# Performance work log

Measured on AMD Instinct MI355X. Metric: run time of the kernel, lower is better.

## Reference

```python
import jax, jax.numpy as jnp
import numpy as np

B, L, D, C = 1, 512, 128, 128  # batch, length, input_dim, channel_dim


def _layernorm(x, w, b, eps=1e-5):
    mu = jnp.mean(x, axis=-1, keepdims=True)
    var = jnp.var(x, axis=-1, keepdims=True)
    return (x - mu) * jax.lax.rsqrt(var + eps) * w + b


def setup_inputs() -> dict:
    key = jax.random.key(0)
    ks = jax.random.split(key, 12)
    s = 0.05  # weight scale ~ xavier for d=128
    f32 = jnp.float32
    return {
        "z": jax.random.normal(ks[0], (B, L, L, D), f32),
        "ln_in_w": jnp.ones((D,), f32), "ln_in_b": jnp.zeros((D,), f32),
        "Wga": jax.random.normal(ks[1], (D, C), f32) * s, "bga": jnp.zeros((C,), f32),
        "Wla": jax.random.normal(ks[2], (D, C), f32) * s, "bla": jnp.zeros((C,), f32),
        "Wgb": jax.random.normal(ks[3], (D, C), f32) * s, "bgb": jnp.zeros((C,), f32),
        "Wlb": jax.random.normal(ks[4], (D, C), f32) * s, "blb": jnp.zeros((C,), f32),
        "ln_o_w": jnp.ones((C,), f32), "ln_o_b": jnp.zeros((C,), f32),
        "Wgo": jax.random.normal(ks[5], (D, D), f32) * s, "bgo": jnp.zeros((D,), f32),
        "Wlo": jax.random.normal(ks[6], (C, D), f32) * s, "blo": jnp.zeros((D,), f32),
    }


def reference(z, ln_in_w, ln_in_b, Wga, bga, Wla, bla, Wgb, bgb, Wlb, blb,
              ln_o_w, ln_o_b, Wgo, bgo, Wlo, blo):
    # z: [B, L, L, D]
    zn = _layernorm(z, ln_in_w, ln_in_b)
    a = jax.nn.sigmoid(zn @ Wga + bga) * (zn @ Wla + bla)   # [B,L,L,C]
    b = jax.nn.sigmoid(zn @ Wgb + bgb) * (zn @ Wlb + blb)   # [B,L,L,C]
    # triangular update (axis=1): per-channel L x L matmul
    # k[b,i,j,c] = sum_m a[b,i,m,c] * b[b,m,j,c]
    k = jnp.einsum('bimc,bmjc->bijc', a, b)
    out = jax.nn.sigmoid(zn @ Wgo + bgo) * (_layernorm(k, ln_o_w, ln_o_b) @ Wlo + blo)
    return out
```

## Files before the change

### kernel.cpp

```cpp
#include <hip/hip_runtime.h>

typedef unsigned short u16;
typedef __attribute__((ext_vector_type(8))) short bf16x8;
typedef __attribute__((ext_vector_type(4))) float f32x4;

#define L_ 512
#define D_ 128
#define LL_ (512*512)
#define LP_ 136
#define TP_ 72

#define WT_OFF 0
#define B2_OFF 98304
#define ZN_OFF (B2_OFF + 1536)
#define AT2_OFF (ZN_OFF + 128*LL_)
#define BT2_OFF (AT2_OFF + 128*LL_)
#define KT2_OFF (BT2_OFF + 128*LL_)
#define WS2_NEED_BYTES ((size_t)(KT2_OFF + 128*LL_) * 2)
#define AT1_OFF (B2_OFF + 1536)
#define BT1_OFF (AT1_OFF + 128*LL_)
#define KT1_OFF (BT1_OFF + 128*LL_)

union U16x8 { uint4 u4; bf16x8 v; u16 s[8]; };
union U16x4 { ushort4 v; u16 s[4]; };

__device__ __forceinline__ u16 f2bf(float f){
  union { float f; unsigned int i; } w; w.f = f;
  unsigned int r = w.i + 0x7FFFu + ((w.i >> 16) & 1u);
  return (u16)(r >> 16);
}
__device__ __forceinline__ float sigm(float x){
  return 1.0f / (1.0f + __expf(-x));
}

__global__ __launch_bounds__(256) void conv_kernel(
    const float* __restrict__ Wga, const float* __restrict__ Wla,
    const float* __restrict__ Wgb, const float* __restrict__ Wlb,
    const float* __restrict__ Wgo, const float* __restrict__ Wlo,
    const float* __restrict__ lnw, const float* __restrict__ lnb,
    const float* __restrict__ onw, const float* __restrict__ onb,
    const float* __restrict__ bga, const float* __restrict__ bla,
    const float* __restrict__ bgb, const float* __restrict__ blb,
    const float* __restrict__ bgo, const float* __restrict__ blo,
    u16* __restrict__ wt, float* __restrict__ bias2)
{
  if (blockIdx.x < 384){
    int idx = blockIdx.x*256 + threadIdx.x;
    int w = idx >> 14, rem = idx & 16383, n = rem >> 7, k = rem & 127;
    const float* src;
    switch (w){
      case 0: src = Wga; break; case 1: src = Wla; break; case 2: src = Wgb; break;
      case 3: src = Wlb; break; case 4: src = Wgo; break; default: src = Wlo;
    }
    float sc = (w == 5) ? onw[k] : lnw[k];
    wt[idx] = f2bf(src[k*128 + n] * sc);
  } else {
    int j = (blockIdx.x - 384)*256 + threadIdx.x;
    int w = j >> 7, n = j & 127;
    const float* src; const float* bs;
    switch (w){
      case 0: src = Wga; bs = bga; break; case 1: src = Wla; bs = bla; break;
      case 2: src = Wgb; bs = bgb; break; case 3: src = Wlb; bs = blb; break;
      case 4: src = Wgo; bs = bgo; break; default: src = Wlo; bs = blo;
    }
    const float* lb = (w == 5) ? onb : lnb;
    float acc = bs[n];
    for (int k = 0; k < 128; ++k) acc += lb[k] * src[k*128 + n];
    bias2[j] = acc;
  }
}

__global__ __launch_bounds__(256) void stageZ_kernel(
    const float* __restrict__ z, u16* __restrict__ zn_g)
{
  const int t = threadIdx.x, r = t >> 1, h = t & 1;
  const int row = blockIdx.x*128 + r;
  const float* zrow = z + (long)row*D_ + h*64;
  float raw[64];
  float sum = 0.f, sq = 0.f;
#pragma unroll
  for (int q = 0; q < 16; ++q){
    float4 v = *(const float4*)(zrow + q*4);
    raw[q*4+0] = v.x; raw[q*4+1] = v.y; raw[q*4+2] = v.z; raw[q*4+3] = v.w;
    sum += v.x + v.y + v.z + v.w;
    sq  += v.x*v.x + v.y*v.y + v.z*v.z + v.w*v.w;
  }
  sum += __shfl_xor(sum, 1, 64);
  sq  += __shfl_xor(sq , 1, 64);
  float mu = sum * (1.f/128.f);
  float rstd = rsqrtf(sq*(1.f/128.f) - mu*mu + 1e-5f);
  u16* orow = zn_g + (long)row*D_ + h*64;
#pragma unroll
  for (int q = 0; q < 8; ++q){
    U16x8 o;
#pragma unroll
    for (int e = 0; e < 8; ++e)
      o.s[e] = f2bf(raw[q*8+e] - mu > 0 ? (raw[q*8+e] - mu)*rstd : (raw[q*8+e] - mu)*rstd);
    *(uint4*)(orow + q*8) = o.u4;
  }
}

__device__ __forceinline__ void gemm128(const u16* znlds, const u16* __restrict__ wtm,
                                        int wm, int wn, int quad, int l16, f32x4 acc[4][4])
{
  bf16x8 bf[4][4];
#pragma unroll
  for (int nt = 0; nt < 4; ++nt){
    int n = wn*64 + nt*16 + l16;
#pragma unroll
    for (int kc = 0; kc < 4; ++kc){
      U16x8 u; u.u4 = *(const uint4*)(wtm + n*128 + kc*32 + quad*8);
      bf[nt][kc] = u.v;
    }
  }
#pragma unroll
  for (int mt = 0; mt < 4; ++mt){
    int row = wm*64 + mt*16 + l16;
    bf16x8 af[4];
#pragma unroll
    for (int kc = 0; kc < 4; ++kc)
      af[kc] = *(const bf16x8*)(znlds + row*LP_ + kc*32 + quad*8);
#pragma unroll
    for (int nt = 0; nt < 4; ++nt)
#pragma unroll
      for (int kc = 0; kc < 4; ++kc)
        acc[mt][nt] = __builtin_amdgcn_mfma_f32_16x16x32_bf16(af[kc], bf[nt][kc], acc[mt][nt], 0, 0, 0);
  }
}

__device__ __forceinline__ void gemm128s(const u16* znS, const u16* __restrict__ wtm,
                                         int wm, int wn, int quad, int l16, f32x4 acc[4][4])
{
  bf16x8 bf[4][4];
#pragma unroll
  for (int nt = 0; nt < 4; ++nt){
    int n = wn*64 + nt*16 + l16;
#pragma unroll
    for (int kc = 0; kc < 4; ++kc){
      U16x8 u; u.u4 = *(const uint4*)(wtm + n*128 + kc*32 + quad*8);
      bf[nt][kc] = u.v;
    }
  }
  const int r7 = l16 & 7;
#pragma unroll
  for (int mt = 0; mt < 4; ++mt){
    int row = wm*64 + mt*16 + l16;
    bf16x8 af[4];
#pragma unroll
    for (int kc = 0; kc < 4; ++kc)
      af[kc] = *(const bf16x8*)(znS + row*128 + (((kc*4 + quad) ^ r7) << 3));
#pragma unroll
    for (int nt = 0; nt < 4; ++nt)
#pragma unroll
      for (int kc = 0; kc < 4; ++kc)
        acc[mt][nt] = __builtin_amdgcn_mfma_f32_16x16x32_bf16(af[kc], bf[nt][kc], acc[mt][nt], 0, 0, 0);
  }
}

__device__ __forceinline__ void gemm64(const u16* alds, const u16* __restrict__ wtm,
                                       int wm, int wn, int quad, int l16, f32x4 acc[2][4])
{
  bf16x8 bf[4][4];
#pragma unroll
  for (int nt = 0; nt < 4; ++nt){
    int n = wn*64 + nt*16 + l16;
#pragma unroll
    for (int kc = 0; kc < 4; ++kc){
      U16x8 u; u.u4 = *(const uint4*)(wtm + n*128 + kc*32 + quad*8);
      bf[nt][kc] = u.v;
    }
  }
#pragma unroll
  for (int mt = 0; mt < 2; ++mt){
    int row = wm*32 + mt*16 + l16;
    bf16x8 af[4];
#pragma unroll
    for (int kc = 0; kc < 4; ++kc)
      af[kc] = *(const bf16x8*)(alds + row*LP_ + kc*32 + quad*8);
#pragma unroll
    for (int nt = 0; nt < 4; ++nt)
#pragma unroll
      for (int kc = 0; kc < 4; ++kc)
        acc[mt][nt] = __builtin_amdgcn_mfma_f32_16x16x32_bf16(af[kc], bf[nt][kc], acc[mt][nt], 0, 0, 0);
  }
}

__global__ __launch_bounds__(256) void stageA2_kernel(
    const u16* __restrict__ zn_g, const u16* __restrict__ wt,
    const float* __restrict__ bias2,
    u16* __restrict__ a_t, u16* __restrict__ b_tt)
{
  __shared__ __align__(16) u16 znS[128*128];

  const int bid = blockIdx.x;
  const int type = bid >> 11;
  const int tile = bid & 2047;
  const int outer = tile >> 2;
  const int seg = tile & 3;

  const int t = threadIdx.x;
  const int r = t >> 1, h = t & 1;
  const int lane = t & 63, wave = t >> 6;
  const int quad = lane >> 4, l16 = lane & 15;
  const int wm = wave & 1, wn = wave >> 1;

  {
    const int lr = lane >> 4, lc = lane & 15;
    const int r7s = (wave*4 + lr) & 7;
    const int cgx = lc ^ r7s;
#pragma unroll
    for (int q = 0; q < 8; ++q){
      int row = q*16 + wave*4 + lr;
      int gpos = (type == 0) ? (outer*L_ + seg*128 + row) : ((seg*128 + row)*L_ + outer);
      __builtin_amdgcn_global_load_lds(
          (const __attribute__((address_space(1))) void*)(zn_g + (long)gpos*D_ + cgx*8),
          (__attribute__((address_space(3))) void*)(&znS[(q*16 + wave*4)*128]),
          16, 0, 0);
    }
  }
  __syncthreads();

  const u16* wg   = wt + (type ? 2 : 0)*16384;
  const u16* wl   = wt + (type ? 3 : 1)*16384;
  const float* bgp = bias2 + (type ? 2 : 0)*128;
  const float* blp = bias2 + (type ? 3 : 1)*128;
  const f32x4 z4 = {0.f, 0.f, 0.f, 0.f};

  f32x4 accG[4][4], accL[4][4];
#pragma unroll
  for (int mt = 0; mt < 4; ++mt)
#pragma unroll
    for (int nt = 0; nt < 4; ++nt){ accG[mt][nt] = z4; accL[mt][nt] = z4; }

  gemm128s(znS, wg, wm, wn, quad, l16, accG);
#pragma unroll
  for (int nt = 0; nt < 4; ++nt){
    float bb = bgp[wn*64 + nt*16 + l16];
#pragma unroll
    for (int mt = 0; mt < 4; ++mt)
#pragma unroll
      for (int e = 0; e < 4; ++e)
        accG[mt][nt][e] = sigm(accG[mt][nt][e] + bb);
  }
  gemm128s(znS, wl, wm, wn, quad, l16, accL);
#pragma unroll
  for (int nt = 0; nt < 4; ++nt){
    float bb = blp[wn*64 + nt*16 + l16];
#pragma unroll
    for (int mt = 0; mt < 4; ++mt)
#pragma unroll
      for (int e = 0; e < 4; ++e)
        accG[mt][nt][e] *= (accL[mt][nt][e] + bb);
  }

  __syncthreads();

  u16* trh = znS;
  u16* dst = type ? b_tt : a_t;
  const int base = outer*L_ + seg*128;
#pragma unroll
  for (int pass = 0; pass < 2; ++pass){
    if (wm == pass){
#pragma unroll
      for (int nt = 0; nt < 4; ++nt){
        int gcol = wn*64 + nt*16 + l16;
#pragma unroll
        for (int mt = 0; mt < 4; ++mt){
          U16x4 pk;
#pragma unroll
          for (int e = 0; e < 4; ++e)
            pk.s[e] = f2bf(accG[mt][nt][e]);
          *(ushort4*)(trh + gcol*TP_ + mt*16 + quad*4) = pk.v;
        }
      }
    }
    __syncthreads();
#pragma unroll
    for (int q = 0; q < 4; ++q){
      uint4 v = *(const uint4*)(trh + r*TP_ + h*32 + q*8);
      *(uint4*)(dst + r*LL_ + base + pass*64 + h*32 + q*8) = v;
    }
    __syncthreads();
  }
}

__global__ __launch_bounds__(256) void stageA_kernel(
    const float* __restrict__ z, const u16* __restrict__ wt,
    const float* __restrict__ bias2,
    u16* __restrict__ a_t, u16* __restrict__ b_tt)
{
  __shared__ __align__(16) u16 smem[128*LP_];
  u16* zn = smem;
  u16* trh = smem;

  const int bid = blockIdx.x;
  const int type = bid >> 11;
  const int tile = bid & 2047;
  const int outer = tile >> 2;
  const int seg = tile & 3;

  const int t = threadIdx.x;
  const int r = t >> 1, h = t & 1;
  const int lane = t & 63, wave = t >> 6;
  const int quad = lane >> 4, l16 = lane & 15;
  const int wm = wave & 1, wn = wave >> 1;

  {
    int gpos = (type == 0) ? (outer*L_ + seg*128 + r) : ((seg*128 + r)*L_ + outer);
    const float* zrow = z + gpos*D_ + h*64;
    float raw[64];
    float sum = 0.f, sq = 0.f;
#pragma unroll
    for (int q = 0; q < 16; ++q){
      float4 v = *(const float4*)(zrow + q*4);
      raw[q*4+0] = v.x; raw[q*4+1] = v.y; raw[q*4+2] = v.z; raw[q*4+3] = v.w;
      sum += v.x + v.y + v.z + v.w;
      sq  += v.x*v.x + v.y*v.y + v.z*v.z + v.w*v.w;
    }
    sum += __shfl_xor(sum, 1, 64);
    sq  += __shfl_xor(sq , 1, 64);
    float mu = sum * (1.f/128.f);
    float rstd = rsqrtf(sq*(1.f/128.f) - mu*mu + 1e-5f);
#pragma unroll
    for (int q = 0; q < 8; ++q){
      U16x8 o;
#pragma unroll
      for (int e = 0; e < 8; ++e)
        o.s[e] = f2bf((raw[q*8+e] - mu)*rstd);
      *(uint4*)(zn + r*LP_ + h*64 + q*8) = o.u4;
    }
  }
  __syncthreads();

  const u16* wg   = wt + (type ? 2 : 0)*16384;
  const u16* wl   = wt + (type ? 3 : 1)*16384;
  const float* bgp = bias2 + (type ? 2 : 0)*128;
  const float* blp = bias2 + (type ? 3 : 1)*128;
  const f32x4 z4 = {0.f, 0.f, 0.f, 0.f};

  f32x4 accG[4][4], accL[4][4];
#pragma unroll
  for (int mt = 0; mt < 4; ++mt)
#pragma unroll
    for (int nt = 0; nt < 4; ++nt){ accG[mt][nt] = z4; accL[mt][nt] = z4; }

  gemm128(zn, wg, wm, wn, quad, l16, accG);
#pragma unroll
  for (int nt = 0; nt < 4; ++nt){
    float bb = bgp[wn*64 + nt*16 + l16];
#pragma unroll
    for (int mt = 0; mt < 4; ++mt)
#pragma unroll
      for (int e = 0; e < 4; ++e)
        accG[mt][nt][e] = sigm(accG[mt][nt][e] + bb);
  }
  gemm128(zn, wl, wm, wn, quad, l16, accL);
#pragma unroll
  for (int nt = 0; nt < 4; ++nt){
    float bb = blp[wn*64 + nt*16 + l16];
#pragma unroll
    for (int mt = 0; mt < 4; ++mt)
#pragma unroll
      for (int e = 0; e < 4; ++e)
        accG[mt][nt][e] *= (accL[mt][nt][e] + bb);
  }

  __syncthreads();

  u16* dst = type ? b_tt : a_t;
  const int base = outer*L_ + seg*128;
#pragma unroll
  for (int pass = 0; pass < 2; ++pass){
    if (wm == pass){
#pragma unroll
      for (int nt = 0; nt < 4; ++nt){
        int gcol = wn*64 + nt*16 + l16;
#pragma unroll
        for (int mt = 0; mt < 4; ++mt){
          U16x4 pk;
#pragma unroll
          for (int e = 0; e < 4; ++e)
            pk.s[e] = f2bf(accG[mt][nt][e]);
          *(ushort4*)(trh + gcol*TP_ + mt*16 + quad*4) = pk.v;
        }
      }
    }
    __syncthreads();
#pragma unroll
    for (int q = 0; q < 4; ++q){
      uint4 v = *(const uint4*)(trh + r*TP_ + h*32 + q*8);
      *(uint4*)(dst + r*LL_ + base + pass*64 + h*32 + q*8) = v;
    }
    __syncthreads();
  }
}

__global__ __launch_bounds__(256) void stageT_kernel(
    const u16* __restrict__ a_t, const u16* __restrict__ b_tt, u16* __restrict__ k_t)
{
  __shared__ __align__(16) u16 As[128*64];
  __shared__ __align__(16) u16 Bs[128*64];
  const int bid = blockIdx.x;
  const int lid = (bid & 7)*256 + (bid >> 3);
  const int c = lid >> 4, it = (lid >> 2) & 3, jt = lid & 3;
  const u16* Ab = a_t + c*LL_ + it*128*L_;
  const u16* Bb = b_tt + c*LL_ + jt*128*L_;
  const int t = threadIdx.x;
  const int lane = t & 63, wave = t >> 6;
  const int quad = lane >> 4, l16 = lane & 15;
  const int wm = wave & 1, wn = wave >> 1;
  const int sr8 = lane >> 3, scl = lane & 7;
  const int cgx = scl ^ sr8;
  const int swz = (l16 & 7) << 3;

  f32x4 acc[4][4];
  const f32x4 z4 = {0.f,0.f,0.f,0.f};
#pragma unroll
  for (int mt = 0; mt < 4; ++mt)
#pragma unroll
    for (int nt = 0; nt < 4; ++nt) acc[mt][nt] = z4;

  for (int kt = 0; kt < 8; ++kt){
    const int k0 = kt*64;
#pragma unroll
    for (int q = 0; q < 4; ++q){
      int row = q*32 + wave*8 + sr8;
      __builtin_amdgcn_global_load_lds(
          (const __attribute__((address_space(1))) void*)(Ab + row*L_ + k0 + cgx*8),
          (__attribute__((address_space(3))) void*)(&As[(q*32 + wave*8)*64]),
          16, 0, 0);
    }
#pragma unroll
    for (int q = 0; q < 4; ++q){
      int row = q*32 + wave*8 + sr8;
      __builtin_amdgcn_global_load_lds(
          (const __attribute__((address_space(1))) void*)(Bb + row*L_ + k0 + cgx*8),
          (__attribute__((address_space(3))) void*)(&Bs[(q*32 + wave*8)*64]),
          16, 0, 0);
    }
    __syncthreads();
    bf16x8 bfr[4][2];
#pragma unroll
    for (int nt = 0; nt < 4; ++nt){
      int brow = wn*64 + nt*16 + l16;
#pragma unroll
      for (int ks = 0; ks < 2; ++ks)
        bfr[nt][ks] = *(const bf16x8*)(Bs + brow*64 + (((ks*4 + quad)*8) ^ swz));
    }
#pragma unroll
    for (int mt = 0; mt < 4; ++mt){
      int arow = wm*64 + mt*16 + l16;
      bf16x8 af[2];
#pragma unroll
      for (int ks = 0; ks < 2; ++ks)
        af[ks] = *(const bf16x8*)(As + arow*64 + (((ks*4 + quad)*8) ^ swz));
#pragma unroll
      for (int nt = 0; nt < 4; ++nt)
#pragma unroll
        for (int ks = 0; ks < 2; ++ks)
          acc[mt][nt] = __builtin_amdgcn_mfma_f32_16x16x32_bf16(af[ks], bfr[nt][ks], acc[mt][nt], 0, 0, 0);
    }
    __syncthreads();
  }

#pragma unroll
  for (int mt = 0; mt < 4; ++mt)
#pragma unroll
    for (int nt = 0; nt < 4; ++nt){
      int gcol = wn*64 + nt*16 + l16;
#pragma unroll
      for (int e = 0; e < 4; ++e){
        int grow = wm*64 + mt*16 + quad*4 + e;
        k_t[c*LL_ + (it*128 + grow)*L_ + jt*128 + gcol] = f2bf(acc[mt][nt][e]);
      }
    }
}

__global__ __launch_bounds__(256) void stageC2_kernel(
    const u16* __restrict__ k_t, const u16* __restrict__ zn_g,
    const u16* __restrict__ wt, const float* __restrict__ bias2,
    float* __restrict__ out)
{
  __shared__ __align__(16) u16 zn2[64*LP_];
  __shared__ __align__(16) u16 kbuf[128*TP_];
  const u16* wtgo = wt + 4*16384;
  const u16* wtlo = wt + 5*16384;
  const float* bgo2 = bias2 + 4*128;
  const float* blo2 = bias2 + 5*128;
  const int bx = blockIdx.x;
  const int pos0 = (bx >> 3)*L_ + (bx & 7)*64;
  const int t = threadIdx.x, r = t >> 1, h = t & 1;
  const int rl4 = t >> 2, qd = t & 3;
  const int lane = t & 63, wave = t >> 6;
  const int quad = lane >> 4, l16 = lane & 15;
  const int wm = wave & 1, wn = wave >> 1;

#pragma unroll
  for (int q = 0; q < 4; ++q)
    *(uint4*)(kbuf + r*TP_ + h*32 + q*8) = *(const uint4*)(k_t + r*LL_ + pos0 + h*32 + q*8);
  __syncthreads();

  {
    float sum = 0.f, sq = 0.f;
    float kv[32];
#pragma unroll
    for (int q = 0; q < 32; ++q){
      union { unsigned int i; float f; } w;
      w.i = ((unsigned int)kbuf[(qd*32 + q)*TP_ + rl4]) << 16;
      kv[q] = w.f; sum += w.f; sq += w.f*w.f;
    }
    sum += __shfl_xor(sum, 1, 64); sq += __shfl_xor(sq, 1, 64);
    sum += __shfl_xor(sum, 2, 64); sq += __shfl_xor(sq, 2, 64);
    float mu = sum*(1.f/128.f);
    float rstd = rsqrtf(sq*(1.f/128.f) - mu*mu + 1e-5f);
#pragma unroll
    for (int q = 0; q < 4; ++q){
      U16x8 o;
#pragma unroll
      for (int e = 0; e < 8; ++e)
        o.s[e] = f2bf((kv[q*8+e] - mu)*rstd);
      *(uint4*)(zn2 + rl4*LP_ + qd*32 + q*8) = o.u4;
    }
  }
  __syncthreads();

  {
    const u16* zr = zn_g + (long)(pos0 + rl4)*D_ + qd*32;
    *(uint4*)(kbuf + rl4*LP_ + qd*32     ) = *(const uint4*)(zr);
    *(uint4*)(kbuf + rl4*LP_ + qd*32 + 8 ) = *(const uint4*)(zr + 8);
    *(uint4*)(kbuf + rl4*LP_ + qd*32 + 16) = *(const uint4*)(zr + 16);
    *(uint4*)(kbuf + rl4*LP_ + qd*32 + 24) = *(const uint4*)(zr + 24);
  }
  __syncthreads();

  f32x4 accK[2][4], accO[2][4];
  const f32x4 z4 = {0.f,0.f,0.f,0.f};
#pragma unroll
  for (int mt = 0; mt < 2; ++mt)
#pragma unroll
    for (int nt = 0; nt < 4; ++nt){ accK[mt][nt] = z4; accO[mt][nt] = z4; }

  gemm64(zn2,  wtlo, wm, wn, quad, l16, accK);
  gemm64(kbuf, wtgo, wm, wn, quad, l16, accO);

#pragma unroll
  for (int nt = 0; nt < 4; ++nt){
    int gcol = wn*64 + nt*16 + l16;
    float bo = bgo2[gcol], bl = blo2[gcol];
#pragma unroll
    for (int mt = 0; mt < 2; ++mt)
#pragma unroll
      for (int e = 0; e < 4; ++e){
        int grow = wm*32 + mt*16 + quad*4 + e;
        float s = sigm(accO[mt][nt][e] + bo);
        out[(pos0 + grow)*D_ + gcol] = s*(accK[mt][nt][e] + bl);
      }
  }
}

__global__ __launch_bounds__(256) void stageC_kernel(
    const u16* __restrict__ k_t, const float* __restrict__ z,
    const u16* __restrict__ wt, const float* __restrict__ bias2,
    float* __restrict__ out)
{
  __shared__ __align__(16) u16 zn2[64*LP_];
  __shared__ __align__(16) u16 kbuf[128*TP_];
  const u16* wtgo = wt + 4*16384;
  const u16* wtlo = wt + 5*16384;
  const float* bgo2 = bias2 + 4*128;
  const float* blo2 = bias2 + 5*128;
  const int bx = blockIdx.x;
  const int pos0 = (bx >> 3)*L_ + (bx & 7)*64;
  const int t = threadIdx.x, r = t >> 1, h = t & 1;
  const int rl4 = t >> 2, qd = t & 3;
  const int lane = t & 63, wave = t >> 6;
  const int quad = lane >> 4, l16 = lane & 15;
  const int wm = wave & 1, wn = wave >> 1;

#pragma unroll
  for (int q = 0; q < 4; ++q)
    *(uint4*)(kbuf + r*TP_ + h*32 + q*8) = *(const uint4*)(k_t + r*LL_ + pos0 + h*32 + q*8);
  __syncthreads();

  {
    float sum = 0.f, sq = 0.f;
    float kv[32];
#pragma unroll
    for (int q = 0; q < 32; ++q){
      union { unsigned int i; float f; } w;
      w.i = ((unsigned int)kbuf[(qd*32 + q)*TP_ + rl4]) << 16;
      kv[q] = w.f; sum += w.f; sq += w.f*w.f;
    }
    sum += __shfl_xor(sum, 1, 64); sq += __shfl_xor(sq, 1, 64);
    sum += __shfl_xor(sum, 2, 64); sq += __shfl_xor(sq, 2, 64);
    float mu = sum*(1.f/128.f);
    float rstd = rsqrtf(sq*(1.f/128.f) - mu*mu + 1e-5f);
#pragma unroll
    for (int q = 0; q < 4; ++q){
      U16x8 o;
#pragma unroll
      for (int e = 0; e < 8; ++e)
        o.s[e] = f2bf((kv[q*8+e] - mu)*rstd);
      *(uint4*)(zn2 + rl4*LP_ + qd*32 + q*8) = o.u4;
    }
  }
  __syncthreads();

  {
    const float* zr = z + (pos0 + rl4)*D_ + qd*32;
    float zv[32];
    float sum = 0.f, sq = 0.f;
#pragma unroll
    for (int q = 0; q < 8; ++q){
      float4 v = *(const float4*)(zr + q*4);
      zv[q*4+0] = v.x; zv[q*4+1] = v.y; zv[q*4+2] = v.z; zv[q*4+3] = v.w;
      sum += v.x + v.y + v.z + v.w;
      sq  += v.x*v.x + v.y*v.y + v.z*v.z + v.w*v.w;
    }
    sum += __shfl_xor(sum, 1, 64); sq += __shfl_xor(sq, 1, 64);
    sum += __shfl_xor(sum, 2, 64); sq += __shfl_xor(sq, 2, 64);
    float mu = sum*(1.f/128.f);
    float rstd = rsqrtf(sq*(1.f/128.f) - mu*mu + 1e-5f);
#pragma unroll
    for (int q = 0; q < 4; ++q){
      U16x8 o;
#pragma unroll
      for (int e = 0; e < 8; ++e)
        o.s[e] = f2bf((zv[q*8+e] - mu)*rstd);
      *(uint4*)(kbuf + rl4*LP_ + qd*32 + q*8) = o.u4;
    }
  }
  __syncthreads();

  f32x4 accK[2][4], accO[2][4];
  const f32x4 z4 = {0.f,0.f,0.f,0.f};
#pragma unroll
  for (int mt = 0; mt < 2; ++mt)
#pragma unroll
    for (int nt = 0; nt < 4; ++nt){ accK[mt][nt] = z4; accO[mt][nt] = z4; }

  gemm64(zn2,  wtlo, wm, wn, quad, l16, accK);
  gemm64(kbuf, wtgo, wm, wn, quad, l16, accO);

#pragma unroll
  for (int nt = 0; nt < 4; ++nt){
    int gcol = wn*64 + nt*16 + l16;
    float bo = bgo2[gcol], bl = blo2[gcol];
#pragma unroll
    for (int mt = 0; mt < 2; ++mt)
#pragma unroll
      for (int e = 0; e < 4; ++e){
        int grow = wm*32 + mt*16 + quad*4 + e;
        float s = sigm(accO[mt][nt][e] + bo);
        out[(pos0 + grow)*D_ + gcol] = s*(accK[mt][nt][e] + bl);
      }
  }
}

extern "C" void kernel_launch(void* const* d_in, const int* in_sizes, int n_in,
                              void* d_out, int out_size, void* d_ws, size_t ws_size,
                              hipStream_t stream)
{
  const float* z   = (const float*)d_in[0];
  const float* lnw = (const float*)d_in[1];
  const float* lnb = (const float*)d_in[2];
  const float* Wga = (const float*)d_in[3];
  const float* bga = (const float*)d_in[4];
  const float* Wla = (const float*)d_in[5];
  const float* bla = (const float*)d_in[6];
  const float* Wgb = (const float*)d_in[7];
  const float* bgb = (const float*)d_in[8];
  const float* Wlb = (const float*)d_in[9];
  const float* blb = (const float*)d_in[10];
  const float* onw = (const float*)d_in[11];
  const float* onb = (const float*)d_in[12];
  const float* Wgo = (const float*)d_in[13];
  const float* bgo = (const float*)d_in[14];
  const float* Wlo = (const float*)d_in[15];
  const float* blo = (const float*)d_in[16];

  u16* ws   = (u16*)d_ws;
  u16* wt   = ws + WT_OFF;
  float* b2 = (float*)(ws + B2_OFF);
  float* out = (float*)d_out;

  conv_kernel<<<387, 256, 0, stream>>>(Wga, Wla, Wgb, Wlb, Wgo, Wlo,
                                       lnw, lnb, onw, onb,
                                       bga, bla, bgb, blb, bgo, blo, wt, b2);

  if (ws_size >= WS2_NEED_BYTES){
    u16* zn_g = ws + ZN_OFF;
    u16* a_t  = ws + AT2_OFF;
    u16* b_tt = ws + BT2_OFF;
    u16* k_t  = ws + KT2_OFF;
    stageZ_kernel<<<2048, 256, 0, stream>>>(z, zn_g);
    stageA2_kernel<<<4096, 256, 0, stream>>>(zn_g, wt, b2, a_t, b_tt);
    stageT_kernel<<<2048, 256, 0, stream>>>(a_t, b_tt, k_t);
    stageC2_kernel<<<4096, 256, 0, stream>>>(k_t, zn_g, wt, b2, out);
  } else {
    u16* a_t  = ws + AT1_OFF;
    u16* b_tt = ws + BT1_OFF;
    u16* k_t  = ws + KT1_OFF;
    stageA_kernel<<<4096, 256, 0, stream>>>(z, wt, b2, a_t, b_tt);
    stageT_kernel<<<2048, 256, 0, stream>>>(a_t, b_tt, k_t);
    stageC_kernel<<<4096, 256, 0, stream>>>(k_t, z, wt, b2, out);
  }
}
```

Baseline: 576.2 us.

## Double-buffer LDS loads in projection and triangular GEMM stages, async loads in output stage

The projection stage now handles two 128-row segments per block and prefetches the second segment into a second LDS buffer while the first is computed, with the grid halved to match. The triangular per-channel GEMM gets double-buffered A/B tiles with explicit vmcnt waits, so the next K-slice load overlaps the current MFMAs. The output stage loads k and zn through asynchronous global-to-LDS copies into swizzled buffers and drops one barrier round. The cost is twice the LDS per block in two kernels, which may lower occupancy, plus hand-written waitcnt counts that must match the number of issued loads.

Measured after the change: 588.2 us. +2.1%, slower.

```diff
diff --git a/kernel.cpp b/kernel.cpp
--- a/kernel.cpp
+++ b/kernel.cpp
@@ -95,7 +95,7 @@
     U16x8 o;
 #pragma unroll
     for (int e = 0; e < 8; ++e)
-      o.s[e] = f2bf(raw[q*8+e] - mu > 0 ? (raw[q*8+e] - mu)*rstd : (raw[q*8+e] - mu)*rstd);
+      o.s[e] = f2bf((raw[q*8+e] - mu)*rstd);
     *(uint4*)(orow + q*8) = o.u4;
   }
 }
@@ -177,6 +177,35 @@
 #pragma unroll
     for (int kc = 0; kc < 4; ++kc)
       af[kc] = *(const bf16x8*)(alds + row*LP_ + kc*32 + quad*8);
+#pragma unroll
+    for (int nt = 0; nt < 4; ++nt)
+#pragma unroll
+      for (int kc = 0; kc < 4; ++kc)
+        acc[mt][nt] = __builtin_amdgcn_mfma_f32_16x16x32_bf16(af[kc], bf[nt][kc], acc[mt][nt], 0, 0, 0);
+  }
+}
+
+__device__ __forceinline__ void gemm64s(const u16* aS, const u16* __restrict__ wtm,
+                                        int wm, int wn, int quad, int l16, f32x4 acc[2][4])
+{
+  bf16x8 bf[4][4];
+#pragma unroll
+  for (int nt = 0; nt < 4; ++nt){
+    int n = wn*64 + nt*16 + l16;
+#pragma unroll
+    for (int kc = 0; kc < 4; ++kc){
+      U16x8 u; u.u4 = *(const uint4*)(wtm + n*128 + kc*32 + quad*8);
+      bf[nt][kc] = u.v;
+    }
+  }
+  const int r7 = l16 & 7;
+#pragma unroll
+  for (int mt = 0; mt < 2; ++mt){
+    int row = wm*32 + mt*16 + l16;
+    bf16x8 af[4];
+#pragma unroll
+    for (int kc = 0; kc < 4; ++kc)
+      af[kc] = *(const bf16x8*)(aS + row*128 + (((kc*4 + quad) ^ r7) << 3));
 #pragma unroll
     for (int nt = 0; nt < 4; ++nt)
 #pragma unroll
@@ -190,7 +219,121 @@
     const float* __restrict__ bias2,
     u16* __restrict__ a_t, u16* __restrict__ b_tt)
 {
-  __shared__ __align__(16) u16 znS[128*128];
+  __shared__ __align__(16) u16 znS[2][128*128];
+
+  const int bid = blockIdx.x;
+  const int type = bid >> 10;
+  const int tile10 = bid & 1023;
+  const int outer = tile10 >> 1;
+  const int sp = (tile10 & 1)*2;
+
+  const int t = threadIdx.x;
+  const int r = t >> 1, h = t & 1;
+  const int lane = t & 63, wave = t >> 6;
+  const int quad = lane >> 4, l16 = lane & 15;
+  const int wm = wave & 1, wn = wave >> 1;
+  const int lr = lane >> 4, lc = lane & 15;
+  const int r7s = (wave*4 + lr) & 7;
+  const int cgx = lc ^ r7s;
+
+  auto stage = [&](int b, int seg){
+#pragma unroll
+    for (int q = 0; q < 8; ++q){
+      int row = q*16 + wave*4 + lr;
+      int gpos = (type == 0) ? (outer*L_ + seg*128 + row) : ((seg*128 + row)*L_ + outer);
+      __builtin_amdgcn_global_load_lds(
+          (const __attribute__((address_space(1))) void*)(zn_g + (long)gpos*D_ + cgx*8),
+          (__attribute__((address_space(3))) void*)(&znS[b][(q*16 + wave*4)*128]),
+          16, 0, 0);
+    }
+  };
+
+  const u16* wg   = wt + (type ? 2 : 0)*16384;
+  const u16* wl   = wt + (type ? 3 : 1)*16384;
+  const float* bgp = bias2 + (type ? 2 : 0)*128;
+  const float* blp = bias2 + (type ? 3 : 1)*128;
+  const f32x4 z4 = {0.f, 0.f, 0.f, 0.f};
+  u16* dst = type ? b_tt : a_t;
+
+  stage(0, sp);
+  for (int it2 = 0; it2 < 2; ++it2){
+    const int seg = sp + it2;
+    if (it2 == 0){
+      stage(1, sp + 1);
+      asm volatile("s_waitcnt vmcnt(8)" ::: "memory");
+    } else {
+      asm volatile("s_waitcnt vmcnt(0)" ::: "memory");
+    }
+    __builtin_amdgcn_s_barrier();
+    asm volatile("" ::: "memory");
+
+    const u16* zn = &znS[it2][0];
+    f32x4 accG[4][4], accL[4][4];
+#pragma unroll
+    for (int mt = 0; mt < 4; ++mt)
+#pragma unroll
+      for (int nt = 0; nt < 4; ++nt){ accG[mt][nt] = z4; accL[mt][nt] = z4; }
+
+    gemm128s(zn, wg, wm, wn, quad, l16, accG);
+#pragma unroll
+    for (int nt = 0; nt < 4; ++nt){
+      float bb = bgp[wn*64 + nt*16 + l16];
+#pragma unroll
+      for (int mt = 0; mt < 4; ++mt)
+#pragma unroll
+        for (int e = 0; e < 4; ++e)
+          accG[mt][nt][e] = sigm(accG[mt][nt][e] + bb);
+    }
+    gemm128s(zn, wl, wm, wn, quad, l16, accL);
+#pragma unroll
+    for (int nt = 0; nt < 4; ++nt){
+      float bb = blp[wn*64 + nt*16 + l16];
+#pragma unroll
+      for (int mt = 0; mt < 4; ++mt)
+#pragma unroll
+        for (int e = 0; e < 4; ++e)
+          accG[mt][nt][e] *= (accL[mt][nt][e] + bb);
+    }
+
+    __syncthreads();
+
+    u16* trh = &znS[it2][0];
+    const int base = outer*L_ + seg*128;
+#pragma unroll
+    for (int pass = 0; pass < 2; ++pass){
+      if (wm == pass){
+#pragma unroll
+        for (int nt = 0; nt < 4; ++nt){
+          int gcol = wn*64 + nt*16 + l16;
+#pragma unroll
+          for (int mt = 0; mt < 4; ++mt){
+            U16x4 pk;
+#pragma unroll
+            for (int e = 0; e < 4; ++e)
+              pk.s[e] = f2bf(accG[mt][nt][e]);
+            *(ushort4*)(trh + gcol*TP_ + mt*16 + quad*4) = pk.v;
+          }
+        }
+      }
+      __syncthreads();
+#pragma unroll
+      for (int q = 0; q < 4; ++q){
+        uint4 v = *(const uint4*)(trh + r*TP_ + h*32 + q*8);
+        *(uint4*)(dst + r*LL_ + base + pass*64 + h*32 + q*8) = v;
+      }
+      __syncthreads();
+    }
+  }
+}
+
+__global__ __launch_bounds__(256) void stageA_kernel(
+    const float* __restrict__ z, const u16* __restrict__ wt,
+    const float* __restrict__ bias2,
+    u16* __restrict__ a_t, u16* __restrict__ b_tt)
+{
+  __shared__ __align__(16) u16 smem[128*LP_];
+  u16* zn = smem;
+  u16* trh = smem;
 
   const int bid = blockIdx.x;
   const int type = bid >> 11;
@@ -205,17 +348,28 @@
   const int wm = wave & 1, wn = wave >> 1;
 
   {
-    const int lr = lane >> 4, lc = lane & 15;
-    const int r7s = (wave*4 + lr) & 7;
-    const int cgx = lc ^ r7s;
+    int gpos = (type == 0) ? (outer*L_ + seg*128 + r) : ((seg*128 + r)*L_ + outer);
+    const float* zrow = z + gpos*D_ + h*64;
+    float raw[64];
+    float sum = 0.f, sq = 0.f;
+#pragma unroll
+    for (int q = 0; q < 16; ++q){
+      float4 v = *(const float4*)(zrow + q*4);
+      raw[q*4+0] = v.x; raw[q*4+1] = v.y; raw[q*4+2] = v.z; raw[q*4+3] = v.w;
+      sum += v.x + v.y + v.z + v.w;
+      sq  += v.x*v.x + v.y*v.y + v.z*v.z + v.w*v.w;
+    }
+    sum += __shfl_xor(sum, 1, 64);
+    sq  += __shfl_xor(sq , 1, 64);
+    float mu = sum * (1.f/128.f);
+    float rstd = rsqrtf(sq*(1.f/128.f) - mu*mu + 1e-5f);
 #pragma unroll
     for (int q = 0; q < 8; ++q){
-      int row = q*16 + wave*4 + lr;
-      int gpos = (type == 0) ? (outer*L_ + seg*128 + row) : ((seg*128 + row)*L_ + outer);
-      __builtin_amdgcn_global_load_lds(
-          (const __attribute__((address_space(1))) void*)(zn_g + (long)gpos*D_ + cgx*8),
-          (__attribute__((address_space(3))) void*)(&znS[(q*16 + wave*4)*128]),
-          16, 0, 0);
+      U16x8 o;
+#pragma unroll
+      for (int e = 0; e < 8; ++e)
+        o.s[e] = f2bf((raw[q*8+e] - mu)*rstd);
+      *(uint4*)(zn + r*LP_ + h*64 + q*8) = o.u4;
     }
   }
   __syncthreads();
@@ -232,7 +386,7 @@
 #pragma unroll
     for (int nt = 0; nt < 4; ++nt){ accG[mt][nt] = z4; accL[mt][nt] = z4; }
 
-  gemm128s(znS, wg, wm, wn, quad, l16, accG);
+  gemm128(zn, wg, wm, wn, quad, l16, accG);
 #pragma unroll
   for (int nt = 0; nt < 4; ++nt){
     float bb = bgp[wn*64 + nt*16 + l16];
@@ -242,7 +396,7 @@
       for (int e = 0; e < 4; ++e)
         accG[mt][nt][e] = sigm(accG[mt][nt][e] + bb);
   }
-  gemm128s(znS, wl, wm, wn, quad, l16, accL);
+  gemm128(zn, wl, wm, wn, quad, l16, accL);
 #pragma unroll
   for (int nt = 0; nt < 4; ++nt){
     float bb = blp[wn*64 + nt*16 + l16];
@@ -255,7 +409,6 @@
 
   __syncthreads();
 
-  u16* trh = znS;
   u16* dst = type ? b_tt : a_t;
   const int base = outer*L_ + seg*128;
 #pragma unroll
@@ -284,122 +437,11 @@
   }
 }
 
-__global__ __launch_bounds__(256) void stageA_kernel(
-    const float* __restrict__ z, const u16* __restrict__ wt,
-    const float* __restrict__ bias2,
-    u16* __restrict__ a_t, u16* __restrict__ b_tt)
-{
-  __shared__ __align__(16) u16 smem[128*LP_];
-  u16* zn = smem;
-  u16* trh = smem;
-
-  const int bid = blockIdx.x;
-  const int type = bid >> 11;
-  const int tile = bid & 2047;
-  const int outer = tile >> 2;
-  const int seg = tile & 3;
-
-  const int t = threadIdx.x;
-  const int r = t >> 1, h = t & 1;
-  const int lane = t & 63, wave = t >> 6;
-  const int quad = lane >> 4, l16 = lane & 15;
-  const int wm = wave & 1, wn = wave >> 1;
-
-  {
-    int gpos = (type == 0) ? (outer*L_ + seg*128 + r) : ((seg*128 + r)*L_ + outer);
-    const float* zrow = z + gpos*D_ + h*64;
-    float raw[64];
-    float sum = 0.f, sq = 0.f;
-#pragma unroll
-    for (int q = 0; q < 16; ++q){
-      float4 v = *(const float4*)(zrow + q*4);
-      raw[q*4+0] = v.x; raw[q*4+1] = v.y; raw[q*4+2] = v.z; raw[q*4+3] = v.w;
-      sum += v.x + v.y + v.z + v.w;
-      sq  += v.x*v.x + v.y*v.y + v.z*v.z + v.w*v.w;
-    }
-    sum += __shfl_xor(sum, 1, 64);
-    sq  += __shfl_xor(sq , 1, 64);
-    float mu = sum * (1.f/128.f);
-    float rstd = rsqrtf(sq*(1.f/128.f) - mu*mu + 1e-5f);
-#pragma unroll
-    for (int q = 0; q < 8; ++q){
-      U16x8 o;
-#pragma unroll
-      for (int e = 0; e < 8; ++e)
-        o.s[e] = f2bf((raw[q*8+e] - mu)*rstd);
-      *(uint4*)(zn + r*LP_ + h*64 + q*8) = o.u4;
-    }
-  }
-  __syncthreads();
-
-  const u16* wg   = wt + (type ? 2 : 0)*16384;
-  const u16* wl   = wt + (type ? 3 : 1)*16384;
-  const float* bgp = bias2 + (type ? 2 : 0)*128;
-  const float* blp = bias2 + (type ? 3 : 1)*128;
-  const f32x4 z4 = {0.f, 0.f, 0.f, 0.f};
-
-  f32x4 accG[4][4], accL[4][4];
-#pragma unroll
-  for (int mt = 0; mt < 4; ++mt)
-#pragma unroll
-    for (int nt = 0; nt < 4; ++nt){ accG[mt][nt] = z4; accL[mt][nt] = z4; }
-
-  gemm128(zn, wg, wm, wn, quad, l16, accG);
-#pragma unroll
-  for (int nt = 0; nt < 4; ++nt){
-    float bb = bgp[wn*64 + nt*16 + l16];
-#pragma unroll
-    for (int mt = 0; mt < 4; ++mt)
-#pragma unroll
-      for (int e = 0; e < 4; ++e)
-        accG[mt][nt][e] = sigm(accG[mt][nt][e] + bb);
-  }
-  gemm128(zn, wl, wm, wn, quad, l16, accL);
-#pragma unroll
-  for (int nt = 0; nt < 4; ++nt){
-    float bb = blp[wn*64 + nt*16 + l16];
-#pragma unroll
-    for (int mt = 0; mt < 4; ++mt)
-#pragma unroll
-      for (int e = 0; e < 4; ++e)
-        accG[mt][nt][e] *= (accL[mt][nt][e] + bb);
-  }
-
-  __syncthreads();
-
-  u16* dst = type ? b_tt : a_t;
-  const int base = outer*L_ + seg*128;
-#pragma unroll
-  for (int pass = 0; pass < 2; ++pass){
-    if (wm == pass){
-#pragma unroll
-      for (int nt = 0; nt < 4; ++nt){
-        int gcol = wn*64 + nt*16 + l16;
-#pragma unroll
-        for (int mt = 0; mt < 4; ++mt){
-          U16x4 pk;
-#pragma unroll
-          for (int e = 0; e < 4; ++e)
-            pk.s[e] = f2bf(accG[mt][nt][e]);
-          *(ushort4*)(trh + gcol*TP_ + mt*16 + quad*4) = pk.v;
-        }
-      }
-    }
-    __syncthreads();
-#pragma unroll
-    for (int q = 0; q < 4; ++q){
-      uint4 v = *(const uint4*)(trh + r*TP_ + h*32 + q*8);
-      *(uint4*)(dst + r*LL_ + base + pass*64 + h*32 + q*8) = v;
-    }
-    __syncthreads();
-  }
-}
-
 __global__ __launch_bounds__(256) void stageT_kernel(
     const u16* __restrict__ a_t, const u16* __restrict__ b_tt, u16* __restrict__ k_t)
 {
-  __shared__ __align__(16) u16 As[128*64];
-  __shared__ __align__(16) u16 Bs[128*64];
+  __shared__ __align__(16) u16 As[2][128*64];
+  __shared__ __align__(16) u16 Bs[2][128*64];
   const int bid = blockIdx.x;
   const int lid = (bid & 7)*256 + (bid >> 3);
   const int c = lid >> 4, it = (lid >> 2) & 3, jt = lid & 3;
@@ -420,14 +462,13 @@
 #pragma unroll
     for (int nt = 0; nt < 4; ++nt) acc[mt][nt] = z4;
 
-  for (int kt = 0; kt < 8; ++kt){
-    const int k0 = kt*64;
+  auto stage = [&](int b, int k0){
 #pragma unroll
     for (int q = 0; q < 4; ++q){
       int row = q*32 + wave*8 + sr8;
       __builtin_amdgcn_global_load_lds(
           (const __attribute__((address_space(1))) void*)(Ab + row*L_ + k0 + cgx*8),
-          (__attribute__((address_space(3))) void*)(&As[(q*32 + wave*8)*64]),
+          (__attribute__((address_space(3))) void*)(&As[b][(q*32 + wave*8)*64]),
           16, 0, 0);
     }
 #pragma unroll
@@ -435,17 +476,31 @@
       int row = q*32 + wave*8 + sr8;
       __builtin_amdgcn_global_load_lds(
           (const __attribute__((address_space(1))) void*)(Bb + row*L_ + k0 + cgx*8),
-          (__attribute__((address_space(3))) void*)(&Bs[(q*32 + wave*8)*64]),
+          (__attribute__((address_space(3))) void*)(&Bs[b][(q*32 + wave*8)*64]),
           16, 0, 0);
     }
-    __syncthreads();
+  };
+
+  stage(0, 0);
+  for (int kt = 0; kt < 8; ++kt){
+    const int cur = kt & 1;
+    if (kt < 7){
+      stage(cur ^ 1, (kt + 1)*64);
+      asm volatile("s_waitcnt vmcnt(8)" ::: "memory");
+    } else {
+      asm volatile("s_waitcnt vmcnt(0)" ::: "memory");
+    }
+    __builtin_amdgcn_s_barrier();
+    asm volatile("" ::: "memory");
+    const u16* Ac = &As[cur][0];
+    const u16* Bc = &Bs[cur][0];
     bf16x8 bfr[4][2];
 #pragma unroll
     for (int nt = 0; nt < 4; ++nt){
       int brow = wn*64 + nt*16 + l16;
 #pragma unroll
       for (int ks = 0; ks < 2; ++ks)
-        bfr[nt][ks] = *(const bf16x8*)(Bs + brow*64 + (((ks*4 + quad)*8) ^ swz));
+        bfr[nt][ks] = *(const bf16x8*)(Bc + brow*64 + (((ks*4 + quad)*8) ^ swz));
     }
 #pragma unroll
     for (int mt = 0; mt < 4; ++mt){
@@ -453,14 +508,16 @@
       bf16x8 af[2];
 #pragma unroll
       for (int ks = 0; ks < 2; ++ks)
-        af[ks] = *(const bf16x8*)(As + arow*64 + (((ks*4 + quad)*8) ^ swz));
+        af[ks] = *(const bf16x8*)(Ac + arow*64 + (((ks*4 + quad)*8) ^ swz));
 #pragma unroll
       for (int nt = 0; nt < 4; ++nt)
 #pragma unroll
         for (int ks = 0; ks < 2; ++ks)
           acc[mt][nt] = __builtin_amdgcn_mfma_f32_16x16x32_bf16(af[ks], bfr[nt][ks], acc[mt][nt], 0, 0, 0);
     }
-    __syncthreads();
+    asm volatile("" ::: "memory");
+    __builtin_amdgcn_s_barrier();
+    asm volatile("" ::: "memory");
   }
 
 #pragma unroll
@@ -481,24 +538,45 @@
     const u16* __restrict__ wt, const float* __restrict__ bias2,
     float* __restrict__ out)
 {
+  __shared__ __align__(16) u16 kl[128*64];
+  __shared__ __align__(16) u16 znp[64*128];
   __shared__ __align__(16) u16 zn2[64*LP_];
-  __shared__ __align__(16) u16 kbuf[128*TP_];
   const u16* wtgo = wt + 4*16384;
   const u16* wtlo = wt + 5*16384;
   const float* bgo2 = bias2 + 4*128;
   const float* blo2 = bias2 + 5*128;
   const int bx = blockIdx.x;
   const int pos0 = (bx >> 3)*L_ + (bx & 7)*64;
-  const int t = threadIdx.x, r = t >> 1, h = t & 1;
+  const int t = threadIdx.x;
   const int rl4 = t >> 2, qd = t & 3;
   const int lane = t & 63, wave = t >> 6;
   const int quad = lane >> 4, l16 = lane & 15;
   const int wm = wave & 1, wn = wave >> 1;
 
 #pragma unroll
-  for (int q = 0; q < 4; ++q)
-    *(uint4*)(kbuf + r*TP_ + h*32 + q*8) = *(const uint4*)(k_t + r*LL_ + pos0 + h*32 + q*8);
-  __syncthreads();
+  for (int q = 0; q < 4; ++q){
+    int base = q*256 + wave*64;
+    int idx = base + lane;
+    int c = idx >> 3, ch = idx & 7;
+    __builtin_amdgcn_global_load_lds(
+        (const __attribute__((address_space(1))) void*)(k_t + (long)c*LL_ + pos0 + ch*8),
+        (__attribute__((address_space(3))) void*)(&kl[base*8]),
+        16, 0, 0);
+  }
+#pragma unroll
+  for (int q = 0; q < 4; ++q){
+    int base = q*256 + wave*64;
+    int idx = base + lane;
+    int j = idx >> 4, ch = idx & 15;
+    int chx = ch ^ (j & 7);
+    __builtin_amdgcn_global_load_lds(
+        (const __attribute__((address_space(1))) void*)(zn_g + (long)(pos0 + j)*D_ + chx*8),
+        (__attribute__((address_space(3))) void*)(&znp[base*8]),
+        16, 0, 0);
+  }
+  asm volatile("s_waitcnt vmcnt(4)" ::: "memory");
+  __builtin_amdgcn_s_barrier();
+  asm volatile("" ::: "memory");
 
   {
     float sum = 0.f, sq = 0.f;
@@ -506,7 +584,7 @@
 #pragma unroll
     for (int q = 0; q < 32; ++q){
       union { unsigned int i; float f; } w;
-      w.i = ((unsigned int)kbuf[(qd*32 + q)*TP_ + rl4]) << 16;
+      w.i = ((unsigned int)kl[(qd*32 + q)*64 + rl4]) << 16;
       kv[q] = w.f; sum += w.f; sq += w.f*w.f;
     }
     sum += __shfl_xor(sum, 1, 64); sq += __shfl_xor(sq, 1, 64);
@@ -524,15 +602,6 @@
   }
   __syncthreads();
 
-  {
-    const u16* zr = zn_g + (long)(pos0 + rl4)*D_ + qd*32;
-    *(uint4*)(kbuf + rl4*LP_ + qd*32     ) = *(const uint4*)(zr);
-    *(uint4*)(kbuf + rl4*LP_ + qd*32 + 8 ) = *(const uint4*)(zr + 8);
-    *(uint4*)(kbuf + rl4*LP_ + qd*32 + 16) = *(const uint4*)(zr + 16);
-    *(uint4*)(kbuf + rl4*LP_ + qd*32 + 24) = *(const uint4*)(zr + 24);
-  }
-  __syncthreads();
-
   f32x4 accK[2][4], accO[2][4];
   const f32x4 z4 = {0.f,0.f,0.f,0.f};
 #pragma unroll
@@ -540,8 +609,8 @@
 #pragma unroll
     for (int nt = 0; nt < 4; ++nt){ accK[mt][nt] = z4; accO[mt][nt] = z4; }
 
-  gemm64(zn2,  wtlo, wm, wn, quad, l16, accK);
-  gemm64(kbuf, wtgo, wm, wn, quad, l16, accO);
+  gemm64 (zn2, wtlo, wm, wn, quad, l16, accK);
+  gemm64s(znp, wtgo, wm, wn, quad, l16, accO);
 
 #pragma unroll
   for (int nt = 0; nt < 4; ++nt){
@@ -694,7 +763,7 @@
     u16* b_tt = ws + BT2_OFF;
     u16* k_t  = ws + KT2_OFF;
     stageZ_kernel<<<2048, 256, 0, stream>>>(z, zn_g);
-    stageA2_kernel<<<4096, 256, 0, stream>>>(zn_g, wt, b2, a_t, b_tt);
+    stageA2_kernel<<<2048, 256, 0, stream>>>(zn_g, wt, b2, a_t, b_tt);
     stageT_kernel<<<2048, 256, 0, stream>>>(a_t, b_tt, k_t);
     stageC2_kernel<<<4096, 256, 0, stream>>>(k_t, zn_g, wt, b2, out);
   } else {
```
